# Kernel tuning notes

Hardware: AMD Instinct MI355X
Metric: run time of the kernel (lower is better)

The kernel has to match this reference:

```python
import jax, jax.numpy as jnp
import numpy as np

N_NODES = 65536
N_EDGES = 1048576
D_IN = 1024
D_HID = 64
N_CLS = 32


def gcn_conv(x, W, b, src, dst, n_nodes):
    """PyG GCNConv: linear transform, then symmetric-normalized aggregation
    with implicit self-loops (fill value 1)."""
    xw = x @ W  # [N, d_out]
    e = src.shape[0]
    # degree over destination index, including the self-loop (+1)
    deg = jax.ops.segment_sum(jnp.ones((e,), xw.dtype), dst, num_segments=n_nodes) + 1.0
    dinv_sqrt = jax.lax.rsqrt(deg)  # deg >= 1, safe
    norm = dinv_sqrt[src] * dinv_sqrt[dst]  # [E]
    agg = jax.ops.segment_sum(xw[src] * norm[:, None], dst, num_segments=n_nodes)
    # self-loop contribution: norm = deg_i^{-1}
    agg = agg + xw * (1.0 / deg)[:, None]
    return agg + b


def setup_inputs() -> dict:
    key = jax.random.key(0)
    k_x, k_e, k_w1, k_b1, k_w2, k_b2 = jax.random.split(key, 6)
    x = jax.random.normal(k_x, (N_NODES, D_IN), dtype=jnp.float32)
    edge_index = jax.random.randint(k_e, (2, N_EDGES), 0, N_NODES, dtype=jnp.int64)
    s1 = 1.0 / np.sqrt(D_IN)
    s2 = 1.0 / np.sqrt(D_HID)
    W1 = jax.random.uniform(k_w1, (D_IN, D_HID), jnp.float32, -s1, s1)
    b1 = jax.random.uniform(k_b1, (D_HID,), jnp.float32, -s1, s1)
    W2 = jax.random.uniform(k_w2, (D_HID, N_CLS), jnp.float32, -s2, s2)
    b2 = jax.random.uniform(k_b2, (N_CLS,), jnp.float32, -s2, s2)
    return {"x": x, "edge_index": edge_index, "W1": W1, "b1": b1, "W2": W2, "b2": b2}


def reference(x, edge_index, W1, b1, W2, b2):
    src, dst = edge_index[0], edge_index[1]
    n = x.shape[0]
    h = gcn_conv(x, W1, b1, src, dst, n)
    h = jax.nn.relu(h)
    # dropout is identity in eval mode
    h = gcn_conv(h, W2, b2, src, dst, n)
    return jax.nn.log_softmax(h, axis=1)
```

## Files before the change

kernel.cpp:

```cpp
#include <hip/hip_runtime.h>
#include <hip/hip_bf16.h>

#define N_NODES 65536
#define D_IN 1024
#define D_HID 64
#define N_CLS 32
#define NBUK 256
#define NEB 1024

typedef short short8 __attribute__((ext_vector_type(8)));
typedef float floatx4 __attribute__((ext_vector_type(4)));

__device__ __forceinline__ unsigned short f2bf(float f) {
  union { float f; unsigned u; } cv; cv.f = f;
  unsigned r = (cv.u + 0x7FFFu + ((cv.u >> 16) & 1u)) >> 16;
  return (unsigned short)r;
}
__device__ __forceinline__ float2 bf2f2(unsigned v) {
  union { unsigned u; float f; } a, b;
  a.u = v << 16;
  b.u = v & 0xFFFF0000u;
  return make_float2(a.f, b.f);
}

__global__ void k_hist(const int* __restrict__ dst, int* __restrict__ H,
                       const float* __restrict__ w1, unsigned short* __restrict__ w1t,
                       int e4) {
  int b = blockIdx.x;
  if (b >= NEB) {
    int i = (b - NEB) * 256 + threadIdx.x;
    int k = i / D_HID, n = i % D_HID;
    w1t[n * D_IN + k] = f2bf(w1[i]);
    return;
  }
  __shared__ int hist[NBUK];
  int t = threadIdx.x;
  hist[t] = 0;
  __syncthreads();
  int i4 = b * 256 + t;
  if (i4 < e4) {
    int4 d = ((const int4*)dst)[i4];
    atomicAdd(&hist[d.x >> 8], 1);
    atomicAdd(&hist[d.y >> 8], 1);
    atomicAdd(&hist[d.z >> 8], 1);
    atomicAdd(&hist[d.w >> 8], 1);
  }
  __syncthreads();
  H[t * NEB + b] = hist[t];
}

__global__ void k_scan_bucket(int* __restrict__ H, int* __restrict__ btot) {
  int bin = blockIdx.x, t = threadIdx.x;
  int4 v = ((int4*)(H + bin * NEB))[t];
  int s0 = v.x, s1 = s0 + v.y, s2 = s1 + v.z, s3 = s2 + v.w;
  __shared__ int s[256];
  s[t] = s3;
  __syncthreads();
  for (int off = 1; off < 256; off <<= 1) {
    int x = (t >= off) ? s[t - off] : 0;
    __syncthreads();
    s[t] += x;
    __syncthreads();
  }
  int excl = s[t] - s3;
  ((int4*)(H + bin * NEB))[t] = make_int4(excl, excl + s0, excl + s1, excl + s2);
  if (t == 255) btot[bin] = excl + s3;
}

__global__ void k_scan_tot(const int* __restrict__ btot, int* __restrict__ btoff,
                           int* __restrict__ rowptr, int e) {
  __shared__ int s[256];
  int t = threadIdx.x;
  int v = btot[t];
  s[t] = v;
  __syncthreads();
  for (int off = 1; off < 256; off <<= 1) {
    int x = (t >= off) ? s[t - off] : 0;
    __syncthreads();
    s[t] += x;
    __syncthreads();
  }
  btoff[t] = s[t] - v;
  if (t == 0) rowptr[N_NODES] = e;
}

__global__ void k_scatter(const int* __restrict__ dst, const int* __restrict__ src,
                          const int* __restrict__ H, const int* __restrict__ btoff,
                          unsigned* __restrict__ pk, int e4) {
  __shared__ int cur[NBUK];
  int b = blockIdx.x, t = threadIdx.x;
  cur[t] = btoff[t] + H[t * NEB + b];
  __syncthreads();
  int i4 = b * 256 + t;
  if (i4 < e4) {
    int4 d = ((const int4*)dst)[i4];
    int4 sv = ((const int4*)src)[i4];
    int p0 = atomicAdd(&cur[d.x >> 8], 1);
    int p1 = atomicAdd(&cur[d.y >> 8], 1);
    int p2 = atomicAdd(&cur[d.z >> 8], 1);
    int p3 = atomicAdd(&cur[d.w >> 8], 1);
    pk[p0] = ((unsigned)(d.x & 255) << 16) | (unsigned)sv.x;
    pk[p1] = ((unsigned)(d.y & 255) << 16) | (unsigned)sv.y;
    pk[p2] = ((unsigned)(d.z & 255) << 16) | (unsigned)sv.z;
    pk[p3] = ((unsigned)(d.w & 255) << 16) | (unsigned)sv.w;
  }
}

__global__ void k_bucket_csr(const unsigned* __restrict__ pk, const int* __restrict__ btoff,
                             const int* __restrict__ btot, int* __restrict__ rowptr,
                             int* __restrict__ csr_src, float* __restrict__ dinv) {
  __shared__ int cnt[NBUK], sc[NBUK], cur[NBUK];
  int bin = blockIdx.x, t = threadIdx.x;
  cnt[t] = 0;
  __syncthreads();
  int beg = btoff[bin], len = btot[bin];
  for (int i = t; i < len; i += 256)
    atomicAdd(&cnt[(pk[beg + i] >> 16) & 255], 1);
  __syncthreads();
  int c = cnt[t];
  sc[t] = c;
  __syncthreads();
  for (int off = 1; off < 256; off <<= 1) {
    int x = (t >= off) ? sc[t - off] : 0;
    __syncthreads();
    sc[t] += x;
    __syncthreads();
  }
  int excl = sc[t] - c;
  int node = bin * 256 + t;
  rowptr[node] = beg + excl;
  dinv[node] = rsqrtf((float)(c + 1));
  cur[t] = excl;
  __syncthreads();
  for (int i = t; i < len; i += 256) {
    unsigned u = pk[beg + i];
    int p = atomicAdd(&cur[(u >> 16) & 255], 1);
    csr_src[beg + p] = (int)(u & 0xFFFFu);
  }
}

__global__ __launch_bounds__(256) void k_gemm1(
    const float* __restrict__ x, const unsigned short* __restrict__ w1t,
    const float* __restrict__ dinv, unsigned short* __restrict__ xw1s) {
  int wave = threadIdx.x >> 6;
  int lane = threadIdx.x & 63;
  int quad = lane >> 4;
  int l16 = lane & 15;
  int rowbase = blockIdx.x * 64 + wave * 16;
  const float* xrow = x + (size_t)(rowbase + l16) * D_IN + quad * 8;
  const unsigned short* bbase = w1t + quad * 8;
  floatx4 acc[4];
#pragma unroll
  for (int nt = 0; nt < 4; nt++) acc[nt] = (floatx4){0.f, 0.f, 0.f, 0.f};
  float4 p0 = *(const float4*)(xrow + 0);
  float4 p1 = *(const float4*)(xrow + 4);
  float4 p2 = *(const float4*)(xrow + 32);
  float4 p3 = *(const float4*)(xrow + 36);
  short8 bf0[4], bf1[4];
#pragma unroll
  for (int nt = 0; nt < 4; nt++) {
    const unsigned short* bp = bbase + (size_t)(nt * 16 + l16) * D_IN;
    bf0[nt] = *(const short8*)(bp);
    bf1[nt] = *(const short8*)(bp + 32);
  }
  for (int k0 = 0; k0 < D_IN; k0 += 64) {
    float4 c0 = p0, c1 = p1, c2 = p2, c3 = p3;
    int kn = (k0 + 64 < D_IN) ? k0 + 64 : k0;
    p0 = *(const float4*)(xrow + kn);
    p1 = *(const float4*)(xrow + kn + 4);
    p2 = *(const float4*)(xrow + kn + 32);
    p3 = *(const float4*)(xrow + kn + 36);
    float av0[8] = {c0.x, c0.y, c0.z, c0.w, c1.x, c1.y, c1.z, c1.w};
    float av1[8] = {c2.x, c2.y, c2.z, c2.w, c3.x, c3.y, c3.z, c3.w};
    short8 af0, af1;
    unsigned* u0 = (unsigned*)&af0;
    unsigned* u1 = (unsigned*)&af1;
#pragma unroll
    for (int j = 0; j < 4; j++) {
      asm("v_cvt_pk_bf16_f32 %0, %1, %2" : "=v"(u0[j]) : "v"(av0[2 * j]), "v"(av0[2 * j + 1]));
      asm("v_cvt_pk_bf16_f32 %0, %1, %2" : "=v"(u1[j]) : "v"(av1[2 * j]), "v"(av1[2 * j + 1]));
    }
#pragma unroll
    for (int nt = 0; nt < 4; nt++)
      acc[nt] = __builtin_amdgcn_mfma_f32_16x16x32_bf16(af0, bf0[nt], acc[nt], 0, 0, 0);
#pragma unroll
    for (int nt = 0; nt < 4; nt++)
      bf0[nt] = *(const short8*)(bbase + (size_t)(nt * 16 + l16) * D_IN + kn);
#pragma unroll
    for (int nt = 0; nt < 4; nt++)
      acc[nt] = __builtin_amdgcn_mfma_f32_16x16x32_bf16(af1, bf1[nt], acc[nt], 0, 0, 0);
#pragma unroll
    for (int nt = 0; nt < 4; nt++)
      bf1[nt] = *(const short8*)(bbase + (size_t)(nt * 16 + l16) * D_IN + kn + 32);
  }
#pragma unroll
  for (int r = 0; r < 4; r++) {
    int row = rowbase + quad * 4 + r;
    float sc = dinv[row];
#pragma unroll
    for (int nt = 0; nt < 4; nt++)
      xw1s[(size_t)row * D_HID + nt * 16 + l16] = f2bf(acc[nt][r] * sc);
  }
}

__global__ __launch_bounds__(256) void k_agg1(const unsigned* __restrict__ xw1s2,
    const int* __restrict__ rowptr, const int* __restrict__ csr_src,
    const float* __restrict__ dinv, const float* __restrict__ b1,
    const float* __restrict__ w2, unsigned short* __restrict__ xw2s) {
  __shared__ float w2s[D_HID * N_CLS];
  for (int i = threadIdx.x; i < D_HID * N_CLS; i += 256) w2s[i] = w2[i];
  __syncthreads();
  int wave = threadIdx.x >> 6;
  int lane = threadIdx.x & 63;
  int h = lane >> 5, l = lane & 31;
  int node = blockIdx.x * 4 + wave;
  float dd = dinv[node];
  int beg = rowptr[node], end = rowptr[node + 1];
  float cx[8], cy[8];
#pragma unroll
  for (int j = 0; j < 8; j++) { cx[j] = 0.f; cy[j] = 0.f; }
  for (int e = beg + h; e < end; e += 16) {
    int idx[8]; bool val[8];
#pragma unroll
    for (int j = 0; j < 8; j++) {
      int ee = e + 2 * j;
      val[j] = ee < end;
      idx[j] = csr_src[val[j] ? ee : beg];
    }
#pragma unroll
    for (int j = 0; j < 8; j++) {
      float2 v = bf2f2(xw1s2[(size_t)idx[j] * 32 + l]);
      cx[j] += val[j] ? v.x : 0.f;
      cy[j] += val[j] ? v.y : 0.f;
    }
  }
  float sx = ((cx[0] + cx[1]) + (cx[2] + cx[3])) + ((cx[4] + cx[5]) + (cx[6] + cx[7]));
  float sy = ((cy[0] + cy[1]) + (cy[2] + cy[3])) + ((cy[4] + cy[5]) + (cy[6] + cy[7]));
  sx += __shfl_xor(sx, 32);
  sy += __shfl_xor(sy, 32);
  float2 self = bf2f2(xw1s2[(size_t)node * 32 + l]);
  float2 bb = ((const float2*)b1)[l];
  float vx = dd * (sx + self.x) + bb.x;
  float vy = dd * (sy + self.y) + bb.y;
  vx = vx > 0.f ? vx : 0.f;
  vy = vy > 0.f ? vy : 0.f;
  int c = lane & 31;
  float p = 0.f;
#pragma unroll
  for (int kk = 0; kk < 32; kk++) {
    int k = h * 32 + kk;
    float hv = (k & 1) ? __shfl(vy, k >> 1) : __shfl(vx, k >> 1);
    p += hv * w2s[k * N_CLS + c];
  }
  p += __shfl_xor(p, 32);
  if (lane < 32) xw2s[(size_t)node * N_CLS + c] = f2bf(p * dd);
}

__global__ __launch_bounds__(256) void k_agg2(const unsigned* __restrict__ xw2s2,
    const int* __restrict__ rowptr, const int* __restrict__ csr_src,
    const float* __restrict__ dinv, const float* __restrict__ b2,
    float* __restrict__ out) {
  int wave = threadIdx.x >> 6;
  int lane = threadIdx.x & 63;
  int q = lane >> 4, l = lane & 15;
  int node = blockIdx.x * 4 + wave;
  float dd = dinv[node];
  int beg = rowptr[node], end = rowptr[node + 1];
  float cx[4], cy[4];
#pragma unroll
  for (int j = 0; j < 4; j++) { cx[j] = 0.f; cy[j] = 0.f; }
  for (int e = beg + q; e < end; e += 16) {
    int idx[4]; bool val[4];
#pragma unroll
    for (int j = 0; j < 4; j++) {
      int ee = e + 4 * j;
      val[j] = ee < end;
      idx[j] = csr_src[val[j] ? ee : beg];
    }
#pragma unroll
    for (int j = 0; j < 4; j++) {
      float2 v = bf2f2(xw2s2[(size_t)idx[j] * 16 + l]);
      cx[j] += val[j] ? v.x : 0.f;
      cy[j] += val[j] ? v.y : 0.f;
    }
  }
  float sx = (cx[0] + cx[1]) + (cx[2] + cx[3]);
  float sy = (cy[0] + cy[1]) + (cy[2] + cy[3]);
  sx += __shfl_xor(sx, 32); sy += __shfl_xor(sy, 32);
  sx += __shfl_xor(sx, 16); sy += __shfl_xor(sy, 16);
  float2 self = bf2f2(xw2s2[(size_t)node * 16 + l]);
  float2 bb = ((const float2*)b2)[l];
  float lx = dd * (sx + self.x) + bb.x;
  float ly = dd * (sy + self.y) + bb.y;
  float m = fmaxf(lx, ly);
#pragma unroll
  for (int o = 8; o > 0; o >>= 1) m = fmaxf(m, __shfl_xor(m, o));
  float s2 = __expf(lx - m) + __expf(ly - m);
#pragma unroll
  for (int o = 8; o > 0; o >>= 1) s2 += __shfl_xor(s2, o);
  float lse = m + __logf(s2);
  if (lane < 16)
    ((float2*)out)[(size_t)node * 16 + l] = make_float2(lx - lse, ly - lse);
}

extern "C" void kernel_launch(void* const* d_in, const int* in_sizes, int n_in,
                              void* d_out, int out_size, void* d_ws, size_t ws_size,
                              hipStream_t stream) {
  (void)n_in; (void)out_size; (void)ws_size;
  const float* x  = (const float*)d_in[0];
  const int*   ei = (const int*)d_in[1];
  const float* w1 = (const float*)d_in[2];
  const float* b1 = (const float*)d_in[3];
  const float* w2 = (const float*)d_in[4];
  const float* b2 = (const float*)d_in[5];
  float* out = (float*)d_out;
  int e = in_sizes[1] / 2;
  const int* src = ei;
  const int* dst = ei + e;

  char* ws = (char*)d_ws;
  int* H              = (int*)(ws + 0x0000000);
  int* btot           = (int*)(ws + 0x0100000);
  int* btoff          = (int*)(ws + 0x0100400);
  int* rowptr         = (int*)(ws + 0x0101000);
  float* dinv         = (float*)(ws + 0x0150000);
  unsigned* pk        = (unsigned*)(ws + 0x0200000);
  int* csr_src        = (int*)(ws + 0x0600000);
  unsigned short* w1t = (unsigned short*)(ws + 0x0A00000);
  unsigned short* xw1s= (unsigned short*)(ws + 0x0A20000);
  unsigned short* xw2s= (unsigned short*)(ws + 0x1220000);

  int e4 = e / 4;
  k_hist       <<<NEB + 256, 256, 0, stream>>>(dst, H, w1, w1t, e4);
  k_scan_bucket<<<NBUK, 256, 0, stream>>>(H, btot);
  k_scan_tot   <<<1, 256, 0, stream>>>(btot, btoff, rowptr, e);
  k_scatter    <<<NEB, 256, 0, stream>>>(dst, src, H, btoff, pk, e4);
  k_bucket_csr <<<NBUK, 256, 0, stream>>>(pk, btoff, btot, rowptr, csr_src, dinv);
  k_gemm1      <<<N_NODES / 64, 256, 0, stream>>>(x, w1t, dinv, xw1s);
  k_agg1       <<<N_NODES / 4, 256, 0, stream>>>((const unsigned*)xw1s, rowptr, csr_src,
                                                 dinv, b1, w2, xw2s);
  k_agg2       <<<N_NODES / 4, 256, 0, stream>>>((const unsigned*)xw2s, rowptr, csr_src,
                                                 dinv, b2, out);
}
```

Before: 493.9 us.

## Fuse edge scatter with GEMM1 and move dinv scaling into aggregation

Edge scatter and the first GEMM now run in one launch, with blocks split by index, so the bandwidth-bound x@W1 GEMM overlaps the CSR bucketing. To allow this, the GEMM no longer scales rows by dinv, since dinv is computed later. Aggregation layer 1 instead gathers dinv[src] per edge and scales the self term. The histogram/scatter now uses 256 blocks of 4096 edges, and the scatter stages bucket-sorted edges in shared memory so global writes are coalesced. The cost is an extra per-edge dinv gather in agg1 and a larger LDS footprint in the scatter blocks.

```diff
diff --git a/kernel.cpp b/kernel.cpp
--- a/kernel.cpp
+++ b/kernel.cpp
@@ -6,7 +6,7 @@
 #define D_HID 64
 #define N_CLS 32
 #define NBUK 256
-#define NEB 1024
+#define NSB 256
 
 typedef short short8 __attribute__((ext_vector_type(8)));
 typedef float floatx4 __attribute__((ext_vector_type(4)));
@@ -23,38 +23,41 @@
   return make_float2(a.f, b.f);
 }
 
-__global__ void k_hist(const int* __restrict__ dst, int* __restrict__ H,
-                       const float* __restrict__ w1, unsigned short* __restrict__ w1t,
-                       int e4) {
-  int b = blockIdx.x;
-  if (b >= NEB) {
-    int i = (b - NEB) * 256 + threadIdx.x;
+__global__ void k_hist_w1t(const int* __restrict__ dst, int* __restrict__ H,
+                           const float* __restrict__ w1, unsigned short* __restrict__ w1t,
+                           int e4) {
+  int b = blockIdx.x, t = threadIdx.x;
+  if (b >= NSB) {
+    int i = (b - NSB) * 256 + t;
     int k = i / D_HID, n = i % D_HID;
     w1t[n * D_IN + k] = f2bf(w1[i]);
     return;
   }
   __shared__ int hist[NBUK];
-  int t = threadIdx.x;
   hist[t] = 0;
   __syncthreads();
-  int i4 = b * 256 + t;
-  if (i4 < e4) {
-    int4 d = ((const int4*)dst)[i4];
-    atomicAdd(&hist[d.x >> 8], 1);
-    atomicAdd(&hist[d.y >> 8], 1);
-    atomicAdd(&hist[d.z >> 8], 1);
-    atomicAdd(&hist[d.w >> 8], 1);
-  }
-  __syncthreads();
-  H[t * NEB + b] = hist[t];
-}
-
-__global__ void k_scan_bucket(int* __restrict__ H, int* __restrict__ btot) {
+  const int4* d4 = (const int4*)dst + b * 1024;
+#pragma unroll
+  for (int p = 0; p < 4; p++) {
+    int i4 = b * 1024 + p * 256 + t;
+    if (i4 < e4) {
+      int4 d = d4[p * 256 + t];
+      atomicAdd(&hist[d.x >> 8], 1);
+      atomicAdd(&hist[d.y >> 8], 1);
+      atomicAdd(&hist[d.z >> 8], 1);
+      atomicAdd(&hist[d.w >> 8], 1);
+    }
+  }
+  __syncthreads();
+  H[b * NBUK + t] = hist[t];
+}
+
+__global__ void k_scan_bin(const int* __restrict__ H, int* __restrict__ Hs,
+                           int* __restrict__ btot) {
   int bin = blockIdx.x, t = threadIdx.x;
-  int4 v = ((int4*)(H + bin * NEB))[t];
-  int s0 = v.x, s1 = s0 + v.y, s2 = s1 + v.z, s3 = s2 + v.w;
+  int v = H[t * NBUK + bin];
   __shared__ int s[256];
-  s[t] = s3;
+  s[t] = v;
   __syncthreads();
   for (int off = 1; off < 256; off <<= 1) {
     int x = (t >= off) ? s[t - off] : 0;
@@ -62,9 +65,8 @@
     s[t] += x;
     __syncthreads();
   }
-  int excl = s[t] - s3;
-  ((int4*)(H + bin * NEB))[t] = make_int4(excl, excl + s0, excl + s1, excl + s2);
-  if (t == 255) btot[bin] = excl + s3;
+  Hs[bin * NSB + t] = s[t] - v;
+  if (t == 255) btot[bin] = s[255];
 }
 
 __global__ void k_scan_tot(const int* __restrict__ btot, int* __restrict__ btoff,
@@ -84,69 +86,73 @@
   if (t == 0) rowptr[N_NODES] = e;
 }
 
-__global__ void k_scatter(const int* __restrict__ dst, const int* __restrict__ src,
-                          const int* __restrict__ H, const int* __restrict__ btoff,
-                          unsigned* __restrict__ pk, int e4) {
-  __shared__ int cur[NBUK];
-  int b = blockIdx.x, t = threadIdx.x;
-  cur[t] = btoff[t] + H[t * NEB + b];
-  __syncthreads();
-  int i4 = b * 256 + t;
-  if (i4 < e4) {
-    int4 d = ((const int4*)dst)[i4];
-    int4 sv = ((const int4*)src)[i4];
-    int p0 = atomicAdd(&cur[d.x >> 8], 1);
-    int p1 = atomicAdd(&cur[d.y >> 8], 1);
-    int p2 = atomicAdd(&cur[d.z >> 8], 1);
-    int p3 = atomicAdd(&cur[d.w >> 8], 1);
-    pk[p0] = ((unsigned)(d.x & 255) << 16) | (unsigned)sv.x;
-    pk[p1] = ((unsigned)(d.y & 255) << 16) | (unsigned)sv.y;
-    pk[p2] = ((unsigned)(d.z & 255) << 16) | (unsigned)sv.z;
-    pk[p3] = ((unsigned)(d.w & 255) << 16) | (unsigned)sv.w;
-  }
-}
-
-__global__ void k_bucket_csr(const unsigned* __restrict__ pk, const int* __restrict__ btoff,
-                             const int* __restrict__ btot, int* __restrict__ rowptr,
-                             int* __restrict__ csr_src, float* __restrict__ dinv) {
-  __shared__ int cnt[NBUK], sc[NBUK], cur[NBUK];
-  int bin = blockIdx.x, t = threadIdx.x;
-  cnt[t] = 0;
-  __syncthreads();
-  int beg = btoff[bin], len = btot[bin];
-  for (int i = t; i < len; i += 256)
-    atomicAdd(&cnt[(pk[beg + i] >> 16) & 255], 1);
-  __syncthreads();
-  int c = cnt[t];
-  sc[t] = c;
-  __syncthreads();
-  for (int off = 1; off < 256; off <<= 1) {
-    int x = (t >= off) ? sc[t - off] : 0;
-    __syncthreads();
-    sc[t] += x;
-    __syncthreads();
-  }
-  int excl = sc[t] - c;
-  int node = bin * 256 + t;
-  rowptr[node] = beg + excl;
-  dinv[node] = rsqrtf((float)(c + 1));
-  cur[t] = excl;
-  __syncthreads();
-  for (int i = t; i < len; i += 256) {
-    unsigned u = pk[beg + i];
-    int p = atomicAdd(&cur[(u >> 16) & 255], 1);
-    csr_src[beg + p] = (int)(u & 0xFFFFu);
-  }
-}
-
-__global__ __launch_bounds__(256) void k_gemm1(
+__global__ __launch_bounds__(256) void k_scatter_gemm1(
+    const int* __restrict__ dst, const int* __restrict__ src,
+    const int* __restrict__ Hs, const int* __restrict__ btoff,
+    unsigned* __restrict__ pk, int e4,
     const float* __restrict__ x, const unsigned short* __restrict__ w1t,
-    const float* __restrict__ dinv, unsigned short* __restrict__ xw1s) {
+    unsigned short* __restrict__ xw1s) {
+  if (blockIdx.x < NSB) {
+    __shared__ int cnt[NBUK], sc[NBUK], cur[NBUK], base2[NBUK];
+    __shared__ unsigned stage[4096];
+    int b = blockIdx.x, t = threadIdx.x;
+    cnt[t] = 0;
+    __syncthreads();
+    const int4* d4 = (const int4*)dst + b * 1024;
+    const int4* s4 = (const int4*)src + b * 1024;
+    int4 dv[4], sv[4]; bool ok[4];
+#pragma unroll
+    for (int p = 0; p < 4; p++) {
+      int i4 = b * 1024 + p * 256 + t;
+      ok[p] = i4 < e4;
+      if (ok[p]) {
+        dv[p] = d4[p * 256 + t];
+        sv[p] = s4[p * 256 + t];
+        atomicAdd(&cnt[dv[p].x >> 8], 1);
+        atomicAdd(&cnt[dv[p].y >> 8], 1);
+        atomicAdd(&cnt[dv[p].z >> 8], 1);
+        atomicAdd(&cnt[dv[p].w >> 8], 1);
+      }
+    }
+    __syncthreads();
+    int c = cnt[t];
+    sc[t] = c;
+    __syncthreads();
+    for (int off = 1; off < 256; off <<= 1) {
+      int xv = (t >= off) ? sc[t - off] : 0;
+      __syncthreads();
+      sc[t] += xv;
+      __syncthreads();
+    }
+    int excl = sc[t] - c;
+    cur[t] = excl;
+    base2[t] = btoff[t] + Hs[t * NSB + b] - excl;
+    __syncthreads();
+    int tot = sc[255];
+#pragma unroll
+    for (int p = 0; p < 4; p++) {
+      if (ok[p]) {
+        int d[4] = {dv[p].x, dv[p].y, dv[p].z, dv[p].w};
+        int s[4] = {sv[p].x, sv[p].y, sv[p].z, sv[p].w};
+#pragma unroll
+        for (int j = 0; j < 4; j++) {
+          int pos = atomicAdd(&cur[d[j] >> 8], 1);
+          stage[pos] = ((unsigned)d[j] << 16) | (unsigned)s[j];
+        }
+      }
+    }
+    __syncthreads();
+    for (int i = t; i < tot; i += 256) {
+      unsigned u = stage[i];
+      pk[base2[u >> 24] + i] = u;
+    }
+    return;
+  }
   int wave = threadIdx.x >> 6;
   int lane = threadIdx.x & 63;
   int quad = lane >> 4;
   int l16 = lane & 15;
-  int rowbase = blockIdx.x * 64 + wave * 16;
+  int rowbase = (blockIdx.x - NSB) * 64 + wave * 16;
   const float* xrow = x + (size_t)(rowbase + l16) * D_IN + quad * 8;
   const unsigned short* bbase = w1t + quad * 8;
   floatx4 acc[4];
@@ -196,10 +202,42 @@
 #pragma unroll
   for (int r = 0; r < 4; r++) {
     int row = rowbase + quad * 4 + r;
-    float sc = dinv[row];
-#pragma unroll
-    for (int nt = 0; nt < 4; nt++)
-      xw1s[(size_t)row * D_HID + nt * 16 + l16] = f2bf(acc[nt][r] * sc);
+#pragma unroll
+    for (int nt = 0; nt < 4; nt++)
+      xw1s[(size_t)row * D_HID + nt * 16 + l16] = f2bf(acc[nt][r]);
+  }
+}
+
+__global__ void k_bucket_csr(const unsigned* __restrict__ pk, const int* __restrict__ btoff,
+                             const int* __restrict__ btot, int* __restrict__ rowptr,
+                             int* __restrict__ csr_src, float* __restrict__ dinv) {
+  __shared__ int cnt[NBUK], sc[NBUK], cur[NBUK];
+  int bin = blockIdx.x, t = threadIdx.x;
+  cnt[t] = 0;
+  __syncthreads();
+  int beg = btoff[bin], len = btot[bin];
+  for (int i = t; i < len; i += 256)
+    atomicAdd(&cnt[(pk[beg + i] >> 16) & 255], 1);
+  __syncthreads();
+  int c = cnt[t];
+  sc[t] = c;
+  __syncthreads();
+  for (int off = 1; off < 256; off <<= 1) {
+    int x = (t >= off) ? sc[t - off] : 0;
+    __syncthreads();
+    sc[t] += x;
+    __syncthreads();
+  }
+  int excl = sc[t] - c;
+  int node = bin * 256 + t;
+  rowptr[node] = beg + excl;
+  dinv[node] = rsqrtf((float)(c + 1));
+  cur[t] = excl;
+  __syncthreads();
+  for (int i = t; i < len; i += 256) {
+    unsigned u = pk[beg + i];
+    int p = atomicAdd(&cur[(u >> 16) & 255], 1);
+    csr_src[beg + p] = (int)(u & 0xFFFFu);
   }
 }
 
@@ -227,11 +265,15 @@
       val[j] = ee < end;
       idx[j] = csr_src[val[j] ? ee : beg];
     }
+    float dv[8];
+#pragma unroll
+    for (int j = 0; j < 8; j++) dv[j] = dinv[idx[j]];
 #pragma unroll
     for (int j = 0; j < 8; j++) {
       float2 v = bf2f2(xw1s2[(size_t)idx[j] * 32 + l]);
-      cx[j] += val[j] ? v.x : 0.f;
-      cy[j] += val[j] ? v.y : 0.f;
+      float w = val[j] ? dv[j] : 0.f;
+      cx[j] += w * v.x;
+      cy[j] += w * v.y;
     }
   }
   float sx = ((cx[0] + cx[1]) + (cx[2] + cx[3])) + ((cx[4] + cx[5]) + (cx[6] + cx[7]));
@@ -240,8 +282,8 @@
   sy += __shfl_xor(sy, 32);
   float2 self = bf2f2(xw1s2[(size_t)node * 32 + l]);
   float2 bb = ((const float2*)b1)[l];
-  float vx = dd * (sx + self.x) + bb.x;
-  float vy = dd * (sy + self.y) + bb.y;
+  float vx = dd * (sx + dd * self.x) + bb.x;
+  float vy = dd * (sy + dd * self.y) + bb.y;
   vx = vx > 0.f ? vx : 0.f;
   vy = vy > 0.f ? vy : 0.f;
   int c = lane & 31;
@@ -320,10 +362,11 @@
 
   char* ws = (char*)d_ws;
   int* H              = (int*)(ws + 0x0000000);
-  int* btot           = (int*)(ws + 0x0100000);
-  int* btoff          = (int*)(ws + 0x0100400);
-  int* rowptr         = (int*)(ws + 0x0101000);
-  float* dinv         = (float*)(ws + 0x0150000);
+  int* Hs             = (int*)(ws + 0x0040000);
+  int* btot           = (int*)(ws + 0x0080000);
+  int* btoff          = (int*)(ws + 0x0080400);
+  int* rowptr         = (int*)(ws + 0x0081000);
+  float* dinv         = (float*)(ws + 0x00D0000);
   unsigned* pk        = (unsigned*)(ws + 0x0200000);
   int* csr_src        = (int*)(ws + 0x0600000);
   unsigned short* w1t = (unsigned short*)(ws + 0x0A00000);
@@ -331,14 +374,14 @@
   unsigned short* xw2s= (unsigned short*)(ws + 0x1220000);
 
   int e4 = e / 4;
-  k_hist       <<<NEB + 256, 256, 0, stream>>>(dst, H, w1, w1t, e4);
-  k_scan_bucket<<<NBUK, 256, 0, stream>>>(H, btot);
-  k_scan_tot   <<<1, 256, 0, stream>>>(btot, btoff, rowptr, e);
-  k_scatter    <<<NEB, 256, 0, stream>>>(dst, src, H, btoff, pk, e4);
-  k_bucket_csr <<<NBUK, 256, 0, stream>>>(pk, btoff, btot, rowptr, csr_src, dinv);
-  k_gemm1      <<<N_NODES / 64, 256, 0, stream>>>(x, w1t, dinv, xw1s);
-  k_agg1       <<<N_NODES / 4, 256, 0, stream>>>((const unsigned*)xw1s, rowptr, csr_src,
-                                                 dinv, b1, w2, xw2s);
-  k_agg2       <<<N_NODES / 4, 256, 0, stream>>>((const unsigned*)xw2s, rowptr, csr_src,
-                                                 dinv, b2, out);
-}
+  k_hist_w1t    <<<NSB + 256, 256, 0, stream>>>(dst, H, w1, w1t, e4);
+  k_scan_bin    <<<NBUK, 256, 0, stream>>>(H, Hs, btot);
+  k_scan_tot    <<<1, 256, 0, stream>>>(btot, btoff, rowptr, e);
+  k_scatter_gemm1<<<NSB + 1024, 256, 0, stream>>>(dst, src, Hs, btoff, pk, e4,
+                                                  x, w1t, xw1s);
+  k_bucket_csr  <<<NBUK, 256, 0, stream>>>(pk, btoff, btot, rowptr, csr_src, dinv);
+  k_agg1        <<<N_NODES / 4, 256, 0, stream>>>((const unsigned*)xw1s, rowptr, csr_src,
+                                                  dinv, b1, w2, xw2s);
+  k_agg2        <<<N_NODES / 4, 256, 0, stream>>>((const unsigned*)xw2s, rowptr, csr_src,
+                                                  dinv, b2, out);
+}
```

New measurement: 489.5 us. About the same (-0.9%).
